# Performance work log

Hardware: AMD Instinct MI355X
Metric: run time of the kernel (lower is better)

The kernel has to match this reference:

```python
import jax, jax.numpy as jnp
import numpy as np

B, L, S, H, E = 2, 2048, 2048, 8, 64

def setup_inputs() -> dict:
    key = jax.random.key(0)
    k1, k2, k3 = jax.random.split(key, 3)
    queries = jax.random.normal(k1, (B, L, H, E), dtype=jnp.float32)
    keys = jax.random.normal(k2, (B, S, H, E), dtype=jnp.float32)
    values = jax.random.normal(k3, (B, S, H, E), dtype=jnp.float32)
    # TriangularCausalMask: True above the diagonal (positions to mask out)
    attn_mask = jnp.broadcast_to(
        jnp.triu(jnp.ones((L, S), dtype=bool), k=1)[None, None], (B, 1, L, S)
    )
    return {"queries": queries, "keys": keys, "values": values, "attn_mask": attn_mask}

def reference(queries, keys, values, attn_mask):
    E_ = queries.shape[-1]
    scale = 1.0 / (E_ ** 0.5)  # self.scale is None -> 1/sqrt(E)
    # scores: [B, H, L, S]
    scores = jnp.einsum('blhe,bshe->bhls', queries, keys)
    scores = jnp.where(attn_mask, -jnp.inf, scores)  # masked_fill_(mask, -inf)
    series = jax.nn.softmax(scale * scores, axis=-1)  # dropout p=0.0 -> identity
    V = jnp.einsum('bhls,bshd->blhd', series, values)
    return V, series
```

## Files before the change

### kernel.cpp

```cpp
#include <hip/hip_runtime.h>

typedef __attribute__((ext_vector_type(8))) short bf16x8;
typedef __attribute__((ext_vector_type(4))) float f32x4;

constexpr int B = 2, L = 2048, S = 2048, H = 8, E = 64;
constexpr int TL = 64;
constexpr int SN = 64;
constexpr int LDK = 72;
constexpr int THREADS = 256;

__device__ __forceinline__ short f2bf(float x) {
  union { float f; unsigned u; } c; c.f = x;
  unsigned r = c.u + 0x7fffu + ((c.u >> 16) & 1u);
  return (short)(r >> 16);
}

__device__ __forceinline__ void stage64(const float* __restrict__ g,
                                        short (* __restrict__ lds)[LDK],
                                        int tid, size_t gstride) {
  const int r = tid >> 2, c = (tid & 3) * 16;
  const float* p = g + (size_t)r * gstride + c;
  float4 v0 = *(const float4*)(p + 0);
  float4 v1 = *(const float4*)(p + 4);
  float4 v2 = *(const float4*)(p + 8);
  float4 v3 = *(const float4*)(p + 12);
  short t[16] = { f2bf(v0.x), f2bf(v0.y), f2bf(v0.z), f2bf(v0.w),
                  f2bf(v1.x), f2bf(v1.y), f2bf(v1.z), f2bf(v1.w),
                  f2bf(v2.x), f2bf(v2.y), f2bf(v2.z), f2bf(v2.w),
                  f2bf(v3.x), f2bf(v3.y), f2bf(v3.z), f2bf(v3.w) };
  *(bf16x8*)&lds[r][c]     = *(bf16x8*)&t[0];
  *(bf16x8*)&lds[r][c + 8] = *(bf16x8*)&t[8];
}

__global__ __launch_bounds__(THREADS, 2)
void attn_tile(const float* __restrict__ Q, const float* __restrict__ K,
               const float* __restrict__ V, float* __restrict__ outV,
               float* __restrict__ outS)
{
  __shared__ __align__(16) short Qs[TL][LDK];
  __shared__ __align__(16) short Ks[SN][LDK];
  __shared__ __align__(16) short Vs[SN][LDK];
  __shared__ __align__(16) short Ps[4][16][LDK];
  __shared__ float inv_lds[TL];

  const int tid  = threadIdx.x;
  const int lane = tid & 63;
  const int wv   = tid >> 6;
  const int quad = lane >> 4;
  const int n16  = lane & 15;

  int t = blockIdx.x;
  t = (t & 1) ? (31 - (t >> 1)) : (t >> 1);
  const int bh = blockIdx.y;
  const int b = bh >> 3, h = bh & 7;
  const int l0 = t * TL;
  const int s_hi = l0 + TL;
  const int nt = s_hi / SN;

  const size_t gstr  = (size_t)H * E;
  const size_t qbase = ((size_t)b * L * H + h) * E;
  const size_t kbase = ((size_t)b * S * H + h) * E;
  const size_t srow  = (size_t)bh * L * S;

  {
    const float4 z = make_float4(0.f, 0.f, 0.f, 0.f);
    for (int r = 0; r < TL; ++r) {
      float4* p = (float4*)(outS + srow + (size_t)(l0 + r) * S);
      for (int s4 = s_hi / 4 + tid; s4 < S / 4; s4 += THREADS)
        p[s4] = z;
    }
  }

  stage64(Q + qbase + (size_t)l0 * gstr, Qs, tid, gstr);
  __syncthreads();

  float rsum[4] = {0.f, 0.f, 0.f, 0.f};
  for (int st = 0; st < nt; ++st) {
    const int s0 = st * SN;
    __syncthreads();
    stage64(K + kbase + (size_t)s0 * gstr, Ks, tid, gstr);
    __syncthreads();

    bf16x8 a0 = *(const bf16x8*)&Qs[wv * 16 + n16][quad * 8];
    bf16x8 a1 = *(const bf16x8*)&Qs[wv * 16 + n16][32 + quad * 8];
#pragma unroll
    for (int nn = 0; nn < 4; ++nn) {
      bf16x8 b0 = *(const bf16x8*)&Ks[nn * 16 + n16][quad * 8];
      bf16x8 b1 = *(const bf16x8*)&Ks[nn * 16 + n16][32 + quad * 8];
      f32x4 acc = {0.f, 0.f, 0.f, 0.f};
      acc = __builtin_amdgcn_mfma_f32_16x16x32_bf16(a0, b0, acc, 0, 0, 0);
      acc = __builtin_amdgcn_mfma_f32_16x16x32_bf16(a1, b1, acc, 0, 0, 0);
#pragma unroll
      for (int r = 0; r < 4; ++r) {
        const int l = l0 + wv * 16 + quad * 4 + r;
        const int s = s0 + nn * 16 + n16;
        rsum[r] += (s <= l) ? __expf(acc[r] * 0.125f) : 0.f;
      }
    }
  }
#pragma unroll
  for (int r = 0; r < 4; ++r)
#pragma unroll
    for (int off = 1; off < 16; off <<= 1)
      rsum[r] += __shfl_xor(rsum[r], off, 64);
  if (n16 == 0)
#pragma unroll
    for (int r = 0; r < 4; ++r)
      inv_lds[wv * 16 + quad * 4 + r] = 1.f / rsum[r];
  __syncthreads();

  float inv_r[4];
#pragma unroll
  for (int r = 0; r < 4; ++r) inv_r[r] = inv_lds[wv * 16 + quad * 4 + r];

  f32x4 oacc[4] = {{0,0,0,0},{0,0,0,0},{0,0,0,0},{0,0,0,0}};
  for (int st = 0; st < nt; ++st) {
    const int s0 = st * SN;
    __syncthreads();
    stage64(K + kbase + (size_t)s0 * gstr, Ks, tid, gstr);
    stage64(V + kbase + (size_t)s0 * gstr, Vs, tid, gstr);
    __syncthreads();

    bf16x8 a0 = *(const bf16x8*)&Qs[wv * 16 + n16][quad * 8];
    bf16x8 a1 = *(const bf16x8*)&Qs[wv * 16 + n16][32 + quad * 8];
#pragma unroll
    for (int nn = 0; nn < 4; ++nn) {
      bf16x8 b0 = *(const bf16x8*)&Ks[nn * 16 + n16][quad * 8];
      bf16x8 b1 = *(const bf16x8*)&Ks[nn * 16 + n16][32 + quad * 8];
      f32x4 acc = {0.f, 0.f, 0.f, 0.f};
      acc = __builtin_amdgcn_mfma_f32_16x16x32_bf16(a0, b0, acc, 0, 0, 0);
      acc = __builtin_amdgcn_mfma_f32_16x16x32_bf16(a1, b1, acc, 0, 0, 0);
#pragma unroll
      for (int r = 0; r < 4; ++r) {
        const int l = l0 + wv * 16 + quad * 4 + r;
        const int s = s0 + nn * 16 + n16;
        float w = (s <= l) ? __expf(acc[r] * 0.125f) * inv_r[r] : 0.f;
        outS[srow + (size_t)l * S + s] = w;
        Ps[wv][quad * 4 + r][nn * 16 + n16] = f2bf(w);
      }
    }
    __syncthreads();

    bf16x8 pa0 = *(const bf16x8*)&Ps[wv][n16][quad * 8];
    bf16x8 pa1 = *(const bf16x8*)&Ps[wv][n16][32 + quad * 8];
#pragma unroll
    for (int nn = 0; nn < 4; ++nn) {
      short vb[16];
#pragma unroll
      for (int j = 0; j < 8; ++j) vb[j]     = Vs[quad * 8 + j][nn * 16 + n16];
#pragma unroll
      for (int j = 0; j < 8; ++j) vb[8 + j] = Vs[32 + quad * 8 + j][nn * 16 + n16];
      oacc[nn] = __builtin_amdgcn_mfma_f32_16x16x32_bf16(pa0, *(bf16x8*)&vb[0], oacc[nn], 0, 0, 0);
      oacc[nn] = __builtin_amdgcn_mfma_f32_16x16x32_bf16(pa1, *(bf16x8*)&vb[8], oacc[nn], 0, 0, 0);
    }
  }

#pragma unroll
  for (int nn = 0; nn < 4; ++nn)
#pragma unroll
    for (int r = 0; r < 4; ++r) {
      const int l = l0 + wv * 16 + quad * 4 + r;
      outV[qbase + (size_t)l * gstr + nn * 16 + n16] = oacc[nn][r];
    }
}

extern "C" void kernel_launch(void* const* d_in, const int* in_sizes, int n_in,
                              void* d_out, int out_size, void* d_ws, size_t ws_size,
                              hipStream_t stream) {
  const float* Q = (const float*)d_in[0];
  const float* K = (const float*)d_in[1];
  const float* V = (const float*)d_in[2];
  float* outV = (float*)d_out;
  float* outS = outV + (size_t)B * L * H * E;
  attn_tile<<<dim3(L / TL, B * H), THREADS, 0, stream>>>(Q, K, V, outV, outS);
}
```

Before: 421.2 us.

## Coalesce score stores via LDS and transpose V with swizzled shared layout

Score probabilities are now staged through the swizzled Ps shared buffer and written to global memory as per-row float4 stores, instead of scattered scalar stores from MFMA fragments. V is stored transposed and XOR-swizzled in LDS so the PV MFMA operands load as vectors rather than sixteen scalar shorts. Float-to-bf16 conversion now uses the packed intrinsic. The emitted probabilities are now bf16-rounded rather than fp32, which lowers output precision.

```diff
diff --git a/kernel.cpp b/kernel.cpp
--- a/kernel.cpp
+++ b/kernel.cpp
@@ -1,4 +1,5 @@
 #include <hip/hip_runtime.h>
+#include <hip/hip_bf16.h>
 
 typedef __attribute__((ext_vector_type(8))) short bf16x8;
 typedef __attribute__((ext_vector_type(4))) float f32x4;
@@ -14,22 +15,45 @@
   unsigned r = c.u + 0x7fffu + ((c.u >> 16) & 1u);
   return (short)(r >> 16);
 }
+__device__ __forceinline__ float bf2f(short s) {
+  union { unsigned u; float f; } c; c.u = ((unsigned)(unsigned short)s) << 16;
+  return c.f;
+}
+
+__device__ __forceinline__ void ld16(const float* __restrict__ p, short* __restrict__ t) {
+  const float4* q = (const float4*)p;
+  float4 v0 = q[0], v1 = q[1], v2 = q[2], v3 = q[3];
+  float vv[16] = { v0.x,v0.y,v0.z,v0.w, v1.x,v1.y,v1.z,v1.w,
+                   v2.x,v2.y,v2.z,v2.w, v3.x,v3.y,v3.z,v3.w };
+#pragma unroll
+  for (int k = 0; k < 8; ++k) {
+    __hip_bfloat162 h = __float22bfloat162_rn(make_float2(vv[2*k], vv[2*k+1]));
+    short2 s2 = *(short2*)&h;
+    t[2*k] = s2.x; t[2*k+1] = s2.y;
+  }
+}
 
 __device__ __forceinline__ void stage64(const float* __restrict__ g,
                                         short (* __restrict__ lds)[LDK],
                                         int tid, size_t gstride) {
   const int r = tid >> 2, c = (tid & 3) * 16;
-  const float* p = g + (size_t)r * gstride + c;
-  float4 v0 = *(const float4*)(p + 0);
-  float4 v1 = *(const float4*)(p + 4);
-  float4 v2 = *(const float4*)(p + 8);
-  float4 v3 = *(const float4*)(p + 12);
-  short t[16] = { f2bf(v0.x), f2bf(v0.y), f2bf(v0.z), f2bf(v0.w),
-                  f2bf(v1.x), f2bf(v1.y), f2bf(v1.z), f2bf(v1.w),
-                  f2bf(v2.x), f2bf(v2.y), f2bf(v2.z), f2bf(v2.w),
-                  f2bf(v3.x), f2bf(v3.y), f2bf(v3.z), f2bf(v3.w) };
+  short t[16];
+  ld16(g + (size_t)r * gstride + c, t);
   *(bf16x8*)&lds[r][c]     = *(bf16x8*)&t[0];
   *(bf16x8*)&lds[r][c + 8] = *(bf16x8*)&t[8];
+}
+
+__device__ __forceinline__ void stageVt(const float* __restrict__ g,
+                                        short (* __restrict__ Vt)[LDK],
+                                        int tid, size_t gstride) {
+  const int s = tid >> 2, c = (tid & 3) * 16;
+  short t[16];
+  ld16(g + (size_t)s * gstride + c, t);
+#pragma unroll
+  for (int i = 0; i < 16; ++i) {
+    const int e = c + i;
+    Vt[e][s ^ (8 * ((e >> 3) & 7))] = t[i];
+  }
 }
 
 __global__ __launch_bounds__(THREADS, 2)
@@ -39,7 +63,7 @@
 {
   __shared__ __align__(16) short Qs[TL][LDK];
   __shared__ __align__(16) short Ks[SN][LDK];
-  __shared__ __align__(16) short Vs[SN][LDK];
+  __shared__ __align__(16) short Vt[E][LDK];
   __shared__ __align__(16) short Ps[4][16][LDK];
   __shared__ float inv_lds[TL];
 
@@ -118,7 +142,7 @@
     const int s0 = st * SN;
     __syncthreads();
     stage64(K + kbase + (size_t)s0 * gstr, Ks, tid, gstr);
-    stage64(V + kbase + (size_t)s0 * gstr, Vs, tid, gstr);
+    stageVt(V + kbase + (size_t)s0 * gstr, Vt, tid, gstr);
     __syncthreads();
 
     bf16x8 a0 = *(const bf16x8*)&Qs[wv * 16 + n16][quad * 8];
@@ -135,23 +159,36 @@
         const int l = l0 + wv * 16 + quad * 4 + r;
         const int s = s0 + nn * 16 + n16;
         float w = (s <= l) ? __expf(acc[r] * 0.125f) * inv_r[r] : 0.f;
-        outS[srow + (size_t)l * S + s] = w;
-        Ps[wv][quad * 4 + r][nn * 16 + n16] = f2bf(w);
+        Ps[wv][quad * 4 + r][(nn * 16 + n16) ^ (8 * quad)] = f2bf(w);
       }
     }
     __syncthreads();
 
-    bf16x8 pa0 = *(const bf16x8*)&Ps[wv][n16][quad * 8];
-    bf16x8 pa1 = *(const bf16x8*)&Ps[wv][n16][32 + quad * 8];
-#pragma unroll
-    for (int nn = 0; nn < 4; ++nn) {
-      short vb[16];
-#pragma unroll
-      for (int j = 0; j < 8; ++j) vb[j]     = Vs[quad * 8 + j][nn * 16 + n16];
-#pragma unroll
-      for (int j = 0; j < 8; ++j) vb[8 + j] = Vs[32 + quad * 8 + j][nn * 16 + n16];
-      oacc[nn] = __builtin_amdgcn_mfma_f32_16x16x32_bf16(pa0, *(bf16x8*)&vb[0], oacc[nn], 0, 0, 0);
-      oacc[nn] = __builtin_amdgcn_mfma_f32_16x16x32_bf16(pa1, *(bf16x8*)&vb[8], oacc[nn], 0, 0, 0);
+    {
+      const int psw = 8 * ((n16 >> 2) & 3);
+      bf16x8 p0 = *(const bf16x8*)&Ps[wv][n16][(quad * 16)     ^ psw];
+      bf16x8 p1 = *(const bf16x8*)&Ps[wv][n16][(quad * 16 + 8) ^ psw];
+      float4 o0 = make_float4(bf2f(p0[0]), bf2f(p0[1]), bf2f(p0[2]), bf2f(p0[3]));
+      float4 o1 = make_float4(bf2f(p0[4]), bf2f(p0[5]), bf2f(p0[6]), bf2f(p0[7]));
+      float4 o2 = make_float4(bf2f(p1[0]), bf2f(p1[1]), bf2f(p1[2]), bf2f(p1[3]));
+      float4 o3 = make_float4(bf2f(p1[4]), bf2f(p1[5]), bf2f(p1[6]), bf2f(p1[7]));
+      float4* dst = (float4*)(outS + srow + (size_t)(l0 + wv * 16 + n16) * S + s0 + quad * 16);
+      dst[0] = o0; dst[1] = o1; dst[2] = o2; dst[3] = o3;
+    }
+
+    {
+      const int psw = 8 * ((n16 >> 2) & 3);
+      bf16x8 pa0 = *(const bf16x8*)&Ps[wv][n16][(quad * 8)      ^ psw];
+      bf16x8 pa1 = *(const bf16x8*)&Ps[wv][n16][(32 + quad * 8) ^ psw];
+#pragma unroll
+      for (int nn = 0; nn < 4; ++nn) {
+        const int e   = nn * 16 + n16;
+        const int vsw = 8 * ((e >> 3) & 7);
+        bf16x8 vb0 = *(const bf16x8*)&Vt[e][(quad * 8)      ^ vsw];
+        bf16x8 vb1 = *(const bf16x8*)&Vt[e][(32 + quad * 8) ^ vsw];
+        oacc[nn] = __builtin_amdgcn_mfma_f32_16x16x32_bf16(pa0, vb0, oacc[nn], 0, 0, 0);
+        oacc[nn] = __builtin_amdgcn_mfma_f32_16x16x32_bf16(pa1, vb1, oacc[nn], 0, 0, 0);
+      }
     }
   }
 
```

After: 409.0 us. 2.9% less time.
